# Kernel optimization log

Hardware: AMD Instinct MI355X
Metric: run time of the kernel (lower is better)

The kernel has to match this reference:

```python
import jax, jax.numpy as jnp
import numpy as np

EPS = 1e-7
NORM_EPS = 1e-12

def _l2norm(x, axis):
    n = jnp.sqrt(jnp.sum(x * x, axis=axis, keepdims=True))
    return x / jnp.maximum(n, NORM_EPS)

def setup_inputs() -> dict:
    key = jax.random.key(0)
    B, M, D, N = 8, 64, 256, 16384
    ks = jax.random.split(key, 10)
    inp = {
        "points": jax.random.normal(ks[0], (B, D, N), jnp.float32),
        "clusters": jax.random.normal(ks[1], (B, M, D), jnp.float32),
        "values": jax.random.normal(ks[2], (B, N, D), jnp.float32),
        "value_clusters": jax.random.normal(ks[3], (B, M, D), jnp.float32),
        # learned params
        "sim_alpha": jnp.ones((M,), jnp.float32),
        "sim_beta": jnp.zeros((M,), jnp.float32),
        "clusters_bias": jnp.zeros((M, D), jnp.float32),
        "Wc": jax.random.normal(ks[4], (D, D), jnp.float32) / np.sqrt(D),
        "bc": jnp.zeros((D,), jnp.float32),
        "value_clusters_bias": jnp.zeros((M, D), jnp.float32),
        "Wv": jax.random.normal(ks[5], (D, D), jnp.float32) / np.sqrt(D),
        "bv": jnp.zeros((D,), jnp.float32),
    }
    return inp

def reference(points, clusters, values, value_clusters,
              sim_alpha, sim_beta, clusters_bias, Wc, bc,
              value_clusters_bias, Wv, bv):
    # per-cluster bias + Linear + SiLU (with_cluster_bias=True, no position)
    c = jax.nn.silu((clusters + clusters_bias) @ Wc.T + bc)            # [B,M,D]
    vc = jax.nn.silu((value_clusters + value_clusters_bias) @ Wv.T + bv)  # [B,M,D]
    # cosine similarity: normalize clusters over last dim, points over dim=-2
    sim = _l2norm(c, -1) @ _l2norm(points, -2)                         # [B,M,N]
    sim = sim_alpha[None, :, None] * sim + sim_beta[None, :, None]
    assignment = jax.nn.softmax(sim, axis=1)                           # over clusters
    agg = (vc + assignment @ values) / (jnp.sum(assignment, axis=-1, keepdims=True) + EPS)  # [B,M,D]
    # x = agg^T @ assignment -> [B,D,N]
    x = jnp.einsum('bmd,bmn->bdn', agg, assignment)
    return x
```

## Files before the change

### kernel.cpp

```cpp
#include <hip/hip_runtime.h>
#include <math.h>

#define BB 8
#define MM 64
#define DD 256
#define NP 16384
#define EPSF 1e-7f
#define NEPS 1e-12f

#define OFF_AT   0u
#define OFF_VC   131072u
#define OFF_AGG  262144u
#define OFF_ASUM 393216u
#define OFF_ASNT 393728u
#define OFF_WCT  8782336u
#define OFF_WVT  8847872u
#define OFF_PART 8913408u

typedef __attribute__((ext_vector_type(8))) short bf16x8;
typedef __attribute__((ext_vector_type(4))) float f32x4;

__global__ __launch_bounds__(256) void k0_transpose(
    const float* __restrict__ Wc, const float* __restrict__ Wv,
    float* __restrict__ ws)
{
    __shared__ float tls[32][33];
    int which = blockIdx.z;
    const float* W = which ? Wv : Wc;
    float* Wt = ws + (which ? OFF_WVT : OFF_WCT);
    int j0 = blockIdx.x * 32, k0 = blockIdx.y * 32;
    int c = threadIdx.x & 31, r0 = threadIdx.x >> 5;
    #pragma unroll
    for (int rr = r0; rr < 32; rr += 8)
        tls[rr][c] = W[(size_t)(j0 + rr) * DD + k0 + c];
    __syncthreads();
    #pragma unroll
    for (int rr = r0; rr < 32; rr += 8)
        Wt[(size_t)(k0 + rr) * DD + j0 + c] = tls[c][rr];
}

__global__ __launch_bounds__(256) void k1_prep(
    const float* __restrict__ clusters, const float* __restrict__ vclusters,
    const float* __restrict__ alpha, const float* __restrict__ cbias,
    const float* __restrict__ bc, const float* __restrict__ vcbias,
    const float* __restrict__ bvv, float* __restrict__ ws)
{
    __shared__ float s_in[16][256];
    __shared__ float wt_s[32][256];
    __shared__ float s_out[16][260];
    __shared__ float s_scale[16];

    int t = threadIdx.x;
    int mt = blockIdx.x, b = blockIdx.y, which = blockIdx.z;
    int m0 = mt * 16;
    const float* inp   = which ? vclusters : clusters;
    const float* ibias = which ? vcbias : cbias;
    const float* obias = which ? bvv : bc;
    const float* Wt = ws + (which ? OFF_WVT : OFF_WCT);

    #pragma unroll
    for (int i = 0; i < 4; i++) {
        int e = i * 1024 + t * 4;
        int r = e >> 8, c = e & 255;
        float4 a  = *(const float4*)&inp[((size_t)(b * MM + m0 + r)) * DD + c];
        float4 bb = *(const float4*)&ibias[(size_t)(m0 + r) * DD + c];
        a.x += bb.x; a.y += bb.y; a.z += bb.z; a.w += bb.w;
        *(float4*)&s_in[r][c] = a;
    }

    int tm = t >> 5, tt = t & 31;
    float acc[2][8];
    #pragma unroll
    for (int i = 0; i < 2; i++)
        #pragma unroll
        for (int q = 0; q < 8; q++) acc[i][q] = 0.f;

    for (int k0 = 0; k0 < DD; k0 += 32) {
        __syncthreads();
        #pragma unroll
        for (int i = 0; i < 8; i++) {
            int e = i * 1024 + t * 4;
            int kd = e >> 8, c = e & 255;
            *(float4*)&wt_s[kd][c] = *(const float4*)&Wt[(size_t)(k0 + kd) * DD + c];
        }
        __syncthreads();
        #pragma unroll
        for (int kd = 0; kd < 32; kd++) {
            float a0 = s_in[tm][k0 + kd];
            float a1 = s_in[tm + 8][k0 + kd];
            float4 b0 = *(const float4*)&wt_s[kd][tt * 4];
            float4 b1 = *(const float4*)&wt_s[kd][128 + tt * 4];
            float bq[8] = {b0.x, b0.y, b0.z, b0.w, b1.x, b1.y, b1.z, b1.w};
            #pragma unroll
            for (int q = 0; q < 8; q++) { acc[0][q] += a0 * bq[q]; acc[1][q] += a1 * bq[q]; }
        }
    }

    #pragma unroll
    for (int q = 0; q < 8; q++) {
        int col = (q < 4) ? (tt * 4 + q) : (128 + tt * 4 + (q - 4));
        float ob = obias[col];
        #pragma unroll
        for (int i = 0; i < 2; i++) {
            int r = tm + i * 8;
            float x = acc[i][q] + ob;
            float s = x / (1.f + __expf(-x));
            s_out[r][col] = s;
        }
    }
    __syncthreads();

    if (which == 0) {
        if (t < 16) {
            float ss = 0.f;
            for (int j = 0; j < 256; j++) { float v = s_out[t][j]; ss += v * v; }
            s_scale[t] = alpha[m0 + t] / fmaxf(sqrtf(ss), NEPS);
        }
        __syncthreads();
        float* At = ws + OFF_AT + (size_t)b * DD * MM + (size_t)t * MM + m0;
        #pragma unroll
        for (int i = 0; i < 16; i++) At[i] = s_out[i][t] * s_scale[i];
    } else {
        float* vc = ws + OFF_VC + (size_t)(b * MM + m0) * DD;
        #pragma unroll
        for (int i = 0; i < 16; i++) vc[(size_t)i * DD + t] = s_out[i][t];
    }
}

__global__ __launch_bounds__(512, 4) void k3_sim(
    const float* __restrict__ points, const float* __restrict__ beta,
    float* __restrict__ ws)
{
    __shared__ __align__(16) unsigned short Ah[64][264];
    __shared__ __align__(16) unsigned short Al[64][264];
    __shared__ float s_red[8][64];
    __shared__ float s_beta[64];

    int t = threadIdx.x;
    int b = blockIdx.y;
    int n0 = blockIdx.x * 256;
    int w = t >> 6;
    int l = t & 63;
    int c = l & 15;
    int g = l >> 4;

    const float* At = ws + OFF_AT + (size_t)b * DD * MM;

    if (t < 64) s_beta[t] = beta[t];

    #pragma unroll
    for (int i = 0; i < 8; i++) {
        int f = i * 512 + t;
        int d = f >> 4, m4 = (f & 15) * 4;
        float4 v = *(const float4*)&At[(size_t)d * MM + m4];
        float xs[4] = {v.x, v.y, v.z, v.w};
        #pragma unroll
        for (int j = 0; j < 4; j++) {
            unsigned u = __float_as_uint(xs[j]);
            float lof = xs[j] - __uint_as_float(u & 0xffff0000u);
            Ah[m4 + j][d] = (unsigned short)(u >> 16);
            Al[m4 + j][d] = (unsigned short)(__float_as_uint(lof) >> 16);
        }
    }
    __syncthreads();

    const float* pb = points + (size_t)b * DD * NP;
    const float* pbase = pb + n0 + w * 32 + c;

    f32x4 acc[4][2];
    #pragma unroll
    for (int am = 0; am < 4; am++)
        #pragma unroll
        for (int an = 0; an < 2; an++)
            acc[am][an] = (f32x4){0.f, 0.f, 0.f, 0.f};

    float sq[2] = {0.f, 0.f};
    float cur[2][8], nxt[2][8];

    #pragma unroll
    for (int an = 0; an < 2; an++)
        #pragma unroll
        for (int i = 0; i < 8; i++)
            cur[an][i] = pbase[(size_t)(g * 8 + i) * NP + an * 16];

    #pragma unroll
    for (int kc = 0; kc < 8; kc++) {
        if (kc < 7) {
            #pragma unroll
            for (int an = 0; an < 2; an++)
                #pragma unroll
                for (int i = 0; i < 8; i++)
                    nxt[an][i] = pbase[(size_t)((kc + 1) * 32 + g * 8 + i) * NP + an * 16];
        }
        union { bf16x8 v; unsigned u[4]; } bh[2], bl[2];
        #pragma unroll
        for (int an = 0; an < 2; an++) {
            #pragma unroll
            for (int p = 0; p < 4; p++) {
                float x0 = cur[an][2 * p], x1 = cur[an][2 * p + 1];
                unsigned u0 = __float_as_uint(x0), u1 = __float_as_uint(x1);
                float l0f = x0 - __uint_as_float(u0 & 0xffff0000u);
                float l1f = x1 - __uint_as_float(u1 & 0xffff0000u);
                bh[an].u[p] = (u0 >> 16) | (u1 & 0xffff0000u);
                bl[an].u[p] = (__float_as_uint(l0f) >> 16) | (__float_as_uint(l1f) & 0xffff0000u);
            }
            #pragma unroll
            for (int i = 0; i < 8; i++) sq[an] += cur[an][i] * cur[an][i];
        }
        #pragma unroll
        for (int am = 0; am < 4; am++) {
            bf16x8 ah = *(const bf16x8*)&Ah[am * 16 + c][kc * 32 + g * 8];
            bf16x8 al = *(const bf16x8*)&Al[am * 16 + c][kc * 32 + g * 8];
            #pragma unroll
            for (int an = 0; an < 2; an++) {
                acc[am][an] = __builtin_amdgcn_mfma_f32_16x16x32_bf16(ah, bh[an].v, acc[am][an], 0, 0, 0);
                acc[am][an] = __builtin_amdgcn_mfma_f32_16x16x32_bf16(ah, bl[an].v, acc[am][an], 0, 0, 0);
                acc[am][an] = __builtin_amdgcn_mfma_f32_16x16x32_bf16(al, bh[an].v, acc[am][an], 0, 0, 0);
            }
        }
        if (kc < 7) {
            #pragma unroll
            for (int an = 0; an < 2; an++)
                #pragma unroll
                for (int i = 0; i < 8; i++) cur[an][i] = nxt[an][i];
        }
    }

    float pinv2[2], cmax[2], csum[2];
    #pragma unroll
    for (int an = 0; an < 2; an++) {
        float s = sq[an];
        s += __shfl_xor(s, 16);
        s += __shfl_xor(s, 32);
        pinv2[an] = 1.f / fmaxf(sqrtf(s), NEPS);
        cmax[an] = -1e30f;
    }

    #pragma unroll
    for (int am = 0; am < 4; am++)
        #pragma unroll
        for (int an = 0; an < 2; an++)
            #pragma unroll
            for (int r = 0; r < 4; r++) {
                float s = acc[am][an][r] * pinv2[an] + s_beta[am * 16 + g * 4 + r];
                acc[am][an][r] = s;
                cmax[an] = fmaxf(cmax[an], s);
            }
    #pragma unroll
    for (int an = 0; an < 2; an++) {
        cmax[an] = fmaxf(cmax[an], __shfl_xor(cmax[an], 16));
        cmax[an] = fmaxf(cmax[an], __shfl_xor(cmax[an], 32));
        csum[an] = 0.f;
    }
    #pragma unroll
    for (int am = 0; am < 4; am++)
        #pragma unroll
        for (int an = 0; an < 2; an++)
            #pragma unroll
            for (int r = 0; r < 4; r++) {
                float e = __expf(acc[am][an][r] - cmax[an]);
                acc[am][an][r] = e;
                csum[an] += e;
            }
    #pragma unroll
    for (int an = 0; an < 2; an++) {
        float s = csum[an];
        s += __shfl_xor(s, 16);
        s += __shfl_xor(s, 32);
        csum[an] = 1.f / s;
    }

    float msum[4][4];
    #pragma unroll
    for (int am = 0; am < 4; am++)
        #pragma unroll
        for (int r = 0; r < 4; r++) msum[am][r] = 0.f;

    float* asnT = ws + OFF_ASNT + (size_t)b * NP * MM;
    int ncol = n0 + w * 32 + c;
    #pragma unroll
    for (int am = 0; am < 4; am++)
        #pragma unroll
        for (int an = 0; an < 2; an++)
            #pragma unroll
            for (int r = 0; r < 4; r++) {
                float v = acc[am][an][r] * csum[an];
                asnT[(size_t)(ncol + an * 16) * MM + am * 16 + g * 4 + r] = v;
                msum[am][r] += v;
            }

    #pragma unroll
    for (int am = 0; am < 4; am++)
        #pragma unroll
        for (int r = 0; r < 4; r++) {
            float s = msum[am][r];
            s += __shfl_xor(s, 1);
            s += __shfl_xor(s, 2);
            s += __shfl_xor(s, 4);
            s += __shfl_xor(s, 8);
            msum[am][r] = s;
        }
    if (c == 0) {
        #pragma unroll
        for (int am = 0; am < 4; am++)
            #pragma unroll
            for (int r = 0; r < 4; r++)
                s_red[w][am * 16 + g * 4 + r] = msum[am][r];
    }
    __syncthreads();
    if (t < 64) {
        float s = 0.f;
        #pragma unroll
        for (int ww = 0; ww < 8; ww++) s += s_red[ww][t];
        atomicAdd(&ws[OFF_ASUM + b * MM + t], s);
    }
}

__global__ __launch_bounds__(512, 4) void k4_av(
    const float* __restrict__ values, float* __restrict__ ws)
{
    __shared__ float Vs[16][256];
    __shared__ float Ast[16][72];
    int t = threadIdx.x;
    int slice = blockIdx.x, b = blockIdx.y;
    int tm = t >> 6, tt = t & 63;
    const float* asnT = ws + OFF_ASNT + (size_t)b * NP * MM;
    const float* vb = values + (size_t)b * NP * DD;

    float acc[8][4];
    #pragma unroll
    for (int i = 0; i < 8; i++)
        #pragma unroll
        for (int q = 0; q < 4; q++) acc[i][q] = 0.f;

    int nbase = slice * 256;
    for (int kc = 0; kc < 16; kc++) {
        int nb = nbase + kc * 16;
        __syncthreads();
        #pragma unroll
        for (int i = 0; i < 2; i++) {
            int f = i * 512 + t;
            int kd = f >> 6, c4 = (f & 63) * 4;
            *(float4*)&Vs[kd][c4] = *(const float4*)&vb[(size_t)(nb + kd) * DD + c4];
        }
        if (t < 256) {
            int kd = t >> 4, me4 = (t & 15) * 4;
            *(float4*)&Ast[kd][me4] = *(const float4*)&asnT[(size_t)(nb + kd) * MM + me4];
        }
        __syncthreads();
        #pragma unroll
        for (int kd = 0; kd < 16; kd++) {
            float4 a0 = *(const float4*)&Ast[kd][tm * 8];
            float4 a1 = *(const float4*)&Ast[kd][tm * 8 + 4];
            float4 b0 = *(const float4*)&Vs[kd][tt * 4];
            float av[8] = {a0.x, a0.y, a0.z, a0.w, a1.x, a1.y, a1.z, a1.w};
            float bq[4] = {b0.x, b0.y, b0.z, b0.w};
            #pragma unroll
            for (int i = 0; i < 8; i++)
                #pragma unroll
                for (int q = 0; q < 4; q++) acc[i][q] += av[i] * bq[q];
        }
    }
    float* part = ws + OFF_PART + ((size_t)slice * BB + b) * MM * DD;
    #pragma unroll
    for (int i = 0; i < 8; i++) {
        int m = tm * 8 + i;
        *(float4*)&part[(size_t)m * DD + tt * 4] =
            make_float4(acc[i][0], acc[i][1], acc[i][2], acc[i][3]);
    }
}

__global__ __launch_bounds__(256) void k5_agg(float* __restrict__ ws)
{
    int bm = blockIdx.x, t = threadIdx.x;
    float r = 1.f / (ws[OFF_ASUM + bm] + EPSF);
    size_t o = (size_t)bm * DD + t;
    const float* part = ws + OFF_PART;
    float s0 = 0.f, s1 = 0.f, s2 = 0.f, s3 = 0.f;
    #pragma unroll 4
    for (int s = 0; s < 64; s += 4) {
        s0 += part[(size_t)(s + 0) * (BB * MM * DD) + o];
        s1 += part[(size_t)(s + 1) * (BB * MM * DD) + o];
        s2 += part[(size_t)(s + 2) * (BB * MM * DD) + o];
        s3 += part[(size_t)(s + 3) * (BB * MM * DD) + o];
    }
    ws[OFF_AGG + o] = (ws[OFF_VC + o] + ((s0 + s1) + (s2 + s3))) * r;
}

__global__ __launch_bounds__(256, 3) void k6_x(
    float* __restrict__ out, const float* __restrict__ ws)
{
    __shared__ float aggs[64][68];
    __shared__ float asns[64][132];
    int t = threadIdx.x;
    int n0 = blockIdx.x * 128, d0 = blockIdx.y * 64, b = blockIdx.z;
    const float* agg = ws + OFF_AGG + (size_t)b * MM * DD;
    const float* asnT = ws + OFF_ASNT + (size_t)b * NP * MM;

    #pragma unroll
    for (int i = 0; i < 4; i++) {
        int f = i * 256 + t;
        int m = f >> 4, c4 = (f & 15) * 4;
        *(float4*)&aggs[m][c4] = *(const float4*)&agg[(size_t)m * DD + d0 + c4];
    }
    #pragma unroll
    for (int s = 0; s < 8; s++) {
        int f = s * 256 + t;
        int nr = f >> 4, fm = f & 15;
        float4 v = *(const float4*)&asnT[(size_t)(n0 + nr) * MM + fm * 4];
        asns[fm * 4 + 0][nr] = v.x; asns[fm * 4 + 1][nr] = v.y;
        asns[fm * 4 + 2][nr] = v.z; asns[fm * 4 + 3][nr] = v.w;
    }
    __syncthreads();

    int td = t >> 5, tn = t & 31;
    float acc[8][4];
    #pragma unroll
    for (int i = 0; i < 8; i++)
        #pragma unroll
        for (int q = 0; q < 4; q++) acc[i][q] = 0.f;

    #pragma unroll 8
    for (int m = 0; m < 64; m++) {
        float4 a0 = *(const float4*)&aggs[m][td * 4];
        float4 a1 = *(const float4*)&aggs[m][32 + td * 4];
        float4 b0 = *(const float4*)&asns[m][tn * 4];
        float av[8] = {a0.x, a0.y, a0.z, a0.w, a1.x, a1.y, a1.z, a1.w};
        float bq[4] = {b0.x, b0.y, b0.z, b0.w};
        #pragma unroll
        for (int i = 0; i < 8; i++)
            #pragma unroll
            for (int q = 0; q < 4; q++) acc[i][q] += av[i] * bq[q];
    }

    float* ob = out + (size_t)b * DD * NP;
    #pragma unroll
    for (int i = 0; i < 8; i++) {
        int d = d0 + ((i < 4) ? (td * 4 + i) : (32 + td * 4 + (i - 4)));
        *(float4*)&ob[(size_t)d * NP + n0 + tn * 4] =
            make_float4(acc[i][0], acc[i][1], acc[i][2], acc[i][3]);
    }
}

extern "C" void kernel_launch(void* const* d_in, const int* in_sizes, int n_in,
                              void* d_out, int out_size, void* d_ws, size_t ws_size,
                              hipStream_t stream) {
    const float* points    = (const float*)d_in[0];
    const float* clusters  = (const float*)d_in[1];
    const float* values    = (const float*)d_in[2];
    const float* vclusters = (const float*)d_in[3];
    const float* alpha     = (const float*)d_in[4];
    const float* beta      = (const float*)d_in[5];
    const float* cbias     = (const float*)d_in[6];
    const float* Wc        = (const float*)d_in[7];
    const float* bc        = (const float*)d_in[8];
    const float* vcbias    = (const float*)d_in[9];
    const float* Wv        = (const float*)d_in[10];
    const float* bvv       = (const float*)d_in[11];
    float* out = (float*)d_out;
    float* ws = (float*)d_ws;

    hipMemsetAsync((char*)d_ws + (size_t)OFF_ASUM * 4, 0, 512 * 4, stream);

    k0_transpose<<<dim3(8, 8, 2), 256, 0, stream>>>(Wc, Wv, ws);
    k1_prep<<<dim3(4, 8, 2), 256, 0, stream>>>(clusters, vclusters, alpha, cbias, bc, vcbias, bvv, ws);
    k3_sim<<<dim3(64, 8), 512, 0, stream>>>(points, beta, ws);
    k4_av<<<dim3(64, 8), 512, 0, stream>>>(values, ws);
    k5_agg<<<dim3(512), 256, 0, stream>>>(ws);
    k6_x<<<dim3(128, 4, 8), 256, 0, stream>>>(out, ws);
}
```

Baseline: 442.8 us.

## Move assignment@values and agg^T@assignment GEMMs to split-bf16 MFMA

Both the A·V aggregation kernel and the final output kernel are rewritten from scalar FP32 FMA loops to bf16 MFMA 16x16x32. Each operand is split into high and low bf16 parts, and three MFMAs per tile keep the result close to FP32 accuracy. The k4 kernel now stages the assignment slice once in LDS, transposed into hi/lo arrays, and streams values from global memory with register double-buffering. k6 is retiled to 64-column n blocks covering all 256 d rows with 512 threads. This adds conversion ALU work and scattered scalar stores in exchange for matrix-core throughput on compute-bound loops.

```diff
diff --git a/kernel.cpp b/kernel.cpp
--- a/kernel.cpp
+++ b/kernel.cpp
@@ -319,55 +319,103 @@
 __global__ __launch_bounds__(512, 4) void k4_av(
     const float* __restrict__ values, float* __restrict__ ws)
 {
-    __shared__ float Vs[16][256];
-    __shared__ float Ast[16][72];
+    __shared__ __align__(16) unsigned short Ah[64][264];
+    __shared__ __align__(16) unsigned short Al[64][264];
+
     int t = threadIdx.x;
     int slice = blockIdx.x, b = blockIdx.y;
-    int tm = t >> 6, tt = t & 63;
+    int w = t >> 6;
+    int l = t & 63;
+    int c = l & 15;
+    int g = l >> 4;
+    int nb = slice * 256;
+
     const float* asnT = ws + OFF_ASNT + (size_t)b * NP * MM;
     const float* vb = values + (size_t)b * NP * DD;
 
-    float acc[8][4];
-    #pragma unroll
-    for (int i = 0; i < 8; i++)
-        #pragma unroll
-        for (int q = 0; q < 4; q++) acc[i][q] = 0.f;
-
-    int nbase = slice * 256;
-    for (int kc = 0; kc < 16; kc++) {
-        int nb = nbase + kc * 16;
-        __syncthreads();
-        #pragma unroll
-        for (int i = 0; i < 2; i++) {
-            int f = i * 512 + t;
-            int kd = f >> 6, c4 = (f & 63) * 4;
-            *(float4*)&Vs[kd][c4] = *(const float4*)&vb[(size_t)(nb + kd) * DD + c4];
-        }
-        if (t < 256) {
-            int kd = t >> 4, me4 = (t & 15) * 4;
-            *(float4*)&Ast[kd][me4] = *(const float4*)&asnT[(size_t)(nb + kd) * MM + me4];
-        }
-        __syncthreads();
-        #pragma unroll
-        for (int kd = 0; kd < 16; kd++) {
-            float4 a0 = *(const float4*)&Ast[kd][tm * 8];
-            float4 a1 = *(const float4*)&Ast[kd][tm * 8 + 4];
-            float4 b0 = *(const float4*)&Vs[kd][tt * 4];
-            float av[8] = {a0.x, a0.y, a0.z, a0.w, a1.x, a1.y, a1.z, a1.w};
-            float bq[4] = {b0.x, b0.y, b0.z, b0.w};
-            #pragma unroll
-            for (int i = 0; i < 8; i++)
+    #pragma unroll
+    for (int i = 0; i < 8; i++) {
+        int f = i * 512 + t;
+        int n = f >> 4, m4 = (f & 15) * 4;
+        float4 v = *(const float4*)&asnT[(size_t)(nb + n) * MM + m4];
+        float xs[4] = {v.x, v.y, v.z, v.w};
+        #pragma unroll
+        for (int j = 0; j < 4; j++) {
+            unsigned u = __float_as_uint(xs[j]);
+            float lof = xs[j] - __uint_as_float(u & 0xffff0000u);
+            Ah[m4 + j][n] = (unsigned short)(u >> 16);
+            Al[m4 + j][n] = (unsigned short)(__float_as_uint(lof) >> 16);
+        }
+    }
+    __syncthreads();
+
+    const float* vbase = vb + (size_t)nb * DD + w * 32 + c;
+
+    f32x4 acc[4][2];
+    #pragma unroll
+    for (int am = 0; am < 4; am++)
+        #pragma unroll
+        for (int an = 0; an < 2; an++)
+            acc[am][an] = (f32x4){0.f, 0.f, 0.f, 0.f};
+
+    float cur[2][8], nxt[2][8];
+    #pragma unroll
+    for (int an = 0; an < 2; an++)
+        #pragma unroll
+        for (int i = 0; i < 8; i++)
+            cur[an][i] = vbase[(size_t)(g * 8 + i) * DD + an * 16];
+
+    #pragma unroll
+    for (int kc = 0; kc < 8; kc++) {
+        if (kc < 7) {
+            #pragma unroll
+            for (int an = 0; an < 2; an++)
                 #pragma unroll
-                for (int q = 0; q < 4; q++) acc[i][q] += av[i] * bq[q];
-        }
-    }
+                for (int i = 0; i < 8; i++)
+                    nxt[an][i] = vbase[(size_t)((kc + 1) * 32 + g * 8 + i) * DD + an * 16];
+        }
+        union { bf16x8 v; unsigned u[4]; } bh[2], bl[2];
+        #pragma unroll
+        for (int an = 0; an < 2; an++) {
+            #pragma unroll
+            for (int p = 0; p < 4; p++) {
+                float x0 = cur[an][2 * p], x1 = cur[an][2 * p + 1];
+                unsigned u0 = __float_as_uint(x0), u1 = __float_as_uint(x1);
+                float l0f = x0 - __uint_as_float(u0 & 0xffff0000u);
+                float l1f = x1 - __uint_as_float(u1 & 0xffff0000u);
+                bh[an].u[p] = (u0 >> 16) | (u1 & 0xffff0000u);
+                bl[an].u[p] = (__float_as_uint(l0f) >> 16) | (__float_as_uint(l1f) & 0xffff0000u);
+            }
+        }
+        #pragma unroll
+        for (int am = 0; am < 4; am++) {
+            bf16x8 ah = *(const bf16x8*)&Ah[am * 16 + c][kc * 32 + g * 8];
+            bf16x8 al = *(const bf16x8*)&Al[am * 16 + c][kc * 32 + g * 8];
+            #pragma unroll
+            for (int an = 0; an < 2; an++) {
+                acc[am][an] = __builtin_amdgcn_mfma_f32_16x16x32_bf16(ah, bh[an].v, acc[am][an], 0, 0, 0);
+                acc[am][an] = __builtin_amdgcn_mfma_f32_16x16x32_bf16(ah, bl[an].v, acc[am][an], 0, 0, 0);
+                acc[am][an] = __builtin_amdgcn_mfma_f32_16x16x32_bf16(al, bh[an].v, acc[am][an], 0, 0, 0);
+            }
+        }
+        if (kc < 7) {
+            #pragma unroll
+            for (int an = 0; an < 2; an++)
+                #pragma unroll
+                for (int i = 0; i < 8; i++) cur[an][i] = nxt[an][i];
+        }
+    }
+
     float* part = ws + OFF_PART + ((size_t)slice * BB + b) * MM * DD;
     #pragma unroll
-    for (int i = 0; i < 8; i++) {
-        int m = tm * 8 + i;
-        *(float4*)&part[(size_t)m * DD + tt * 4] =
-            make_float4(acc[i][0], acc[i][1], acc[i][2], acc[i][3]);
-    }
+    for (int am = 0; am < 4; am++)
+        #pragma unroll
+        for (int an = 0; an < 2; an++)
+            #pragma unroll
+            for (int r = 0; r < 4; r++) {
+                int m = am * 16 + g * 4 + r;
+                part[(size_t)m * DD + w * 32 + an * 16 + c] = acc[am][an][r];
+            }
 }
 
 __global__ __launch_bounds__(256) void k5_agg(float* __restrict__ ws)
@@ -387,59 +435,90 @@
     ws[OFF_AGG + o] = (ws[OFF_VC + o] + ((s0 + s1) + (s2 + s3))) * r;
 }
 
-__global__ __launch_bounds__(256, 3) void k6_x(
+__global__ __launch_bounds__(512, 4) void k6_x(
     float* __restrict__ out, const float* __restrict__ ws)
 {
-    __shared__ float aggs[64][68];
-    __shared__ float asns[64][132];
+    __shared__ __align__(16) unsigned short Ah[256][72];
+    __shared__ __align__(16) unsigned short Al[256][72];
+
     int t = threadIdx.x;
-    int n0 = blockIdx.x * 128, d0 = blockIdx.y * 64, b = blockIdx.z;
+    int n0 = blockIdx.x * 64, b = blockIdx.y;
+    int w = t >> 6;
+    int l = t & 63;
+    int c = l & 15;
+    int g = l >> 4;
+    int dq = w >> 1, nh = w & 1;
+
     const float* agg = ws + OFF_AGG + (size_t)b * MM * DD;
     const float* asnT = ws + OFF_ASNT + (size_t)b * NP * MM;
 
     #pragma unroll
-    for (int i = 0; i < 4; i++) {
-        int f = i * 256 + t;
-        int m = f >> 4, c4 = (f & 15) * 4;
-        *(float4*)&aggs[m][c4] = *(const float4*)&agg[(size_t)m * DD + d0 + c4];
-    }
-    #pragma unroll
-    for (int s = 0; s < 8; s++) {
-        int f = s * 256 + t;
-        int nr = f >> 4, fm = f & 15;
-        float4 v = *(const float4*)&asnT[(size_t)(n0 + nr) * MM + fm * 4];
-        asns[fm * 4 + 0][nr] = v.x; asns[fm * 4 + 1][nr] = v.y;
-        asns[fm * 4 + 2][nr] = v.z; asns[fm * 4 + 3][nr] = v.w;
-    }
+    for (int i = 0; i < 8; i++) {
+        int f = i * 512 + t;
+        int m = f >> 6, d4 = (f & 63) * 4;
+        float4 v = *(const float4*)&agg[(size_t)m * DD + d4];
+        float xs[4] = {v.x, v.y, v.z, v.w};
+        #pragma unroll
+        for (int j = 0; j < 4; j++) {
+            unsigned u = __float_as_uint(xs[j]);
+            float lof = xs[j] - __uint_as_float(u & 0xffff0000u);
+            Ah[d4 + j][m] = (unsigned short)(u >> 16);
+            Al[d4 + j][m] = (unsigned short)(__float_as_uint(lof) >> 16);
+        }
+    }
+
+    union { bf16x8 v; unsigned u[4]; } bh[2][2], bl[2][2];
+    #pragma unroll
+    for (int kc = 0; kc < 2; kc++)
+        #pragma unroll
+        for (int an = 0; an < 2; an++) {
+            const float* src = &asnT[(size_t)(n0 + nh * 32 + an * 16 + c) * MM + kc * 32 + g * 8];
+            float4 v0 = *(const float4*)src;
+            float4 v1 = *(const float4*)(src + 4);
+            float xs[8] = {v0.x, v0.y, v0.z, v0.w, v1.x, v1.y, v1.z, v1.w};
+            #pragma unroll
+            for (int p = 0; p < 4; p++) {
+                float x0 = xs[2 * p], x1 = xs[2 * p + 1];
+                unsigned u0 = __float_as_uint(x0), u1 = __float_as_uint(x1);
+                float l0f = x0 - __uint_as_float(u0 & 0xffff0000u);
+                float l1f = x1 - __uint_as_float(u1 & 0xffff0000u);
+                bh[kc][an].u[p] = (u0 >> 16) | (u1 & 0xffff0000u);
+                bl[kc][an].u[p] = (__float_as_uint(l0f) >> 16) | (__float_as_uint(l1f) & 0xffff0000u);
+            }
+        }
     __syncthreads();
 
-    int td = t >> 5, tn = t & 31;
-    float acc[8][4];
-    #pragma unroll
-    for (int i = 0; i < 8; i++)
-        #pragma unroll
-        for (int q = 0; q < 4; q++) acc[i][q] = 0.f;
-
-    #pragma unroll 8
-    for (int m = 0; m < 64; m++) {
-        float4 a0 = *(const float4*)&aggs[m][td * 4];
-        float4 a1 = *(const float4*)&aggs[m][32 + td * 4];
-        float4 b0 = *(const float4*)&asns[m][tn * 4];
-        float av[8] = {a0.x, a0.y, a0.z, a0.w, a1.x, a1.y, a1.z, a1.w};
-        float bq[4] = {b0.x, b0.y, b0.z, b0.w};
-        #pragma unroll
-        for (int i = 0; i < 8; i++)
-            #pragma unroll
-            for (int q = 0; q < 4; q++) acc[i][q] += av[i] * bq[q];
-    }
+    f32x4 acc[4][2];
+    #pragma unroll
+    for (int am = 0; am < 4; am++)
+        #pragma unroll
+        for (int an = 0; an < 2; an++)
+            acc[am][an] = (f32x4){0.f, 0.f, 0.f, 0.f};
+
+    #pragma unroll
+    for (int kc = 0; kc < 2; kc++)
+        #pragma unroll
+        for (int am = 0; am < 4; am++) {
+            bf16x8 ah = *(const bf16x8*)&Ah[dq * 64 + am * 16 + c][kc * 32 + g * 8];
+            bf16x8 al = *(const bf16x8*)&Al[dq * 64 + am * 16 + c][kc * 32 + g * 8];
+            #pragma unroll
+            for (int an = 0; an < 2; an++) {
+                acc[am][an] = __builtin_amdgcn_mfma_f32_16x16x32_bf16(ah, bh[kc][an].v, acc[am][an], 0, 0, 0);
+                acc[am][an] = __builtin_amdgcn_mfma_f32_16x16x32_bf16(ah, bl[kc][an].v, acc[am][an], 0, 0, 0);
+                acc[am][an] = __builtin_amdgcn_mfma_f32_16x16x32_bf16(al, bh[kc][an].v, acc[am][an], 0, 0, 0);
+            }
+        }
 
     float* ob = out + (size_t)b * DD * NP;
     #pragma unroll
-    for (int i = 0; i < 8; i++) {
-        int d = d0 + ((i < 4) ? (td * 4 + i) : (32 + td * 4 + (i - 4)));
-        *(float4*)&ob[(size_t)d * NP + n0 + tn * 4] =
-            make_float4(acc[i][0], acc[i][1], acc[i][2], acc[i][3]);
-    }
+    for (int am = 0; am < 4; am++)
+        #pragma unroll
+        for (int an = 0; an < 2; an++)
+            #pragma unroll
+            for (int r = 0; r < 4; r++) {
+                int d = dq * 64 + am * 16 + g * 4 + r;
+                ob[(size_t)d * NP + n0 + nh * 32 + an * 16 + c] = acc[am][an][r];
+            }
 }
 
 extern "C" void kernel_launch(void* const* d_in, const int* in_sizes, int n_in,
@@ -467,5 +546,5 @@
     k3_sim<<<dim3(64, 8), 512, 0, stream>>>(points, beta, ws);
     k4_av<<<dim3(64, 8), 512, 0, stream>>>(values, ws);
     k5_agg<<<dim3(512), 256, 0, stream>>>(ws);
-    k6_x<<<dim3(128, 4, 8), 256, 0, stream>>>(out, ws);
-}
+    k6_x<<<dim3(256, 8), 512, 0, stream>>>(out, ws);
+}
```

New measurement: 440.4 us. About the same (-0.5%).
